# Performance work log

Measured on AMD Instinct MI355X. Metric: run time of the kernel, lower is better.

## Reference

```python
import jax, jax.numpy as jnp
import numpy as np

PS = 8          # patch_size
NF = 64         # num_feat
HEADS = 1
HW = 64         # hard-coded spatial size (Fold output_size=(64,64))
DIM = PS * PS * NF          # 4096
HID = DIM // HEADS          # 4096
NPATCH = (HW // PS) ** 2    # 64


def conv2d(x, w, b, groups=1):
    # x: [N,C,H,W], w: [O, C//groups, 3, 3], padding=1 stride=1 == SAME
    y = jax.lax.conv_general_dilated(
        x, w, window_strides=(1, 1), padding='SAME',
        dimension_numbers=('NCHW', 'OIHW', 'NCHW'),
        feature_group_count=groups)
    return y + b[None, :, None, None]


def unfold(x):
    # nn.Unfold(kernel=PS, stride=PS): [N,C,64,64] -> [N, C*PS*PS, NPATCH]
    N, C = x.shape[0], x.shape[1]
    g = HW // PS
    x = x.reshape(N, C, g, PS, g, PS)          # [N,C,gh,pi,gw,pj]
    x = x.transpose(0, 1, 3, 5, 2, 4)          # [N,C,pi,pj,gh,gw]
    return x.reshape(N, C * PS * PS, g * g)


def fold(y):
    # nn.Fold(output=(64,64), kernel=PS, stride=PS): inverse of unfold (non-overlapping)
    N = y.shape[0]
    g = HW // PS
    y = y.reshape(N, NF, PS, PS, g, g)         # [N,C,pi,pj,gh,gw]
    y = y.transpose(0, 1, 4, 2, 5, 3)          # [N,C,gh,pi,gw,pj]
    return y.reshape(N, NF, HW, HW)


def setup_inputs() -> dict:
    key = jax.random.key(0)
    ks = jax.random.split(key, 9)
    b, t = 4, 16
    x = jax.random.normal(ks[0], (b, t, NF, HW, HW), dtype=jnp.float32)
    s_dw = 1.0 / np.sqrt(9.0)          # depthwise: fan_in = 1*3*3
    s_fc = 1.0 / np.sqrt(NF * 9.0)     # full conv: fan_in = 64*3*3
    qw = jax.random.normal(ks[1], (NF, 1, 3, 3), jnp.float32) * s_dw
    qb = jax.random.normal(ks[2], (NF,), jnp.float32) * 0.01
    kw = jax.random.normal(ks[3], (NF, 1, 3, 3), jnp.float32) * s_dw
    kb = jax.random.normal(ks[4], (NF,), jnp.float32) * 0.01
    vw = jax.random.normal(ks[5], (NF, NF, 3, 3), jnp.float32) * s_fc
    vb = jax.random.normal(ks[6], (NF,), jnp.float32) * 0.01
    cw = jax.random.normal(ks[7], (NF, NF, 3, 3), jnp.float32) * s_fc
    cb = jax.random.normal(ks[8], (NF,), jnp.float32) * 0.01
    return {"x": x, "qw": qw, "qb": qb, "kw": kw, "kb": kb,
            "vw": vw, "vb": vb, "cw": cw, "cb": cb}


def reference(x, qw, qb, kw, kb, vw, vb, cw, cb):
    b, t, c, h, w = x.shape
    H, d, n = HEADS, HID, NPATCH
    xf = x.reshape(b * t, c, h, w)
    q = conv2d(xf, qw, qb, groups=NF)   # depthwise
    k = conv2d(xf, kw, kb, groups=NF)   # depthwise
    v = conv2d(xf, vw, vb)              # full conv
    # unfold -> [b,t,H,d,n] -> [b,H,d,t*n]
    def to_tokens(z):
        z = unfold(z).reshape(b, t, H, d, n)
        return z.transpose(0, 2, 3, 1, 4).reshape(b, H, d, t * n)
    uq, uk, uv = to_tokens(q), to_tokens(k), to_tokens(v)
    attn = jnp.einsum('bhdi,bhdj->bhij', uq, uk) * (d ** -0.5)
    attn = jax.nn.softmax(attn, axis=-1)
    ax = jnp.einsum('bhij,bhdj->bhid', attn, uv)          # [b,H,t*n,d]
    ax = ax.reshape(b, H, t, n, d).transpose(0, 2, 1, 4, 3)  # [b,t,H,d,n]
    ax = ax.reshape(b * t, DIM, n)
    feat = fold(ax)                                        # [b*t,C,64,64]
    out = conv2d(feat, cw, cb).reshape(x.shape)
    return out + x
```

## Files before the change

kernel.cpp:

```cpp
#include <hip/hip_runtime.h>

typedef unsigned short u16;
typedef unsigned int   u32;

typedef __bf16 bf16_t;
typedef bf16_t bf16x8 __attribute__((ext_vector_type(8)));
typedef float  f32x4  __attribute__((ext_vector_type(4)));

__device__ __forceinline__ float bf2f(u16 h) { return __uint_as_float(((u32)h) << 16); }
__device__ __forceinline__ u16 f2bf(float f) {
    u32 u = __float_as_uint(f);
    u32 r = u + 0x7fffu + ((u >> 16) & 1u);
    return (u16)(r >> 16);
}
__device__ __forceinline__ void unpack2(u32 v, float& a, float& b) {
    a = __uint_as_float(v << 16);
    b = __uint_as_float(v & 0xffff0000u);
}


__global__ __launch_bounds__(256) void dwconv_qk(
    const float* __restrict__ x, const float* __restrict__ qw, const float* __restrict__ qb,
    const float* __restrict__ kw, const float* __restrict__ kb,
    u16* __restrict__ qtok, u16* __restrict__ ktok)
{
    __shared__ float ts[64][65];
    int img = blockIdx.x >> 6, c = blockIdx.x & 63;
    int tid = threadIdx.x;
    const float* xp = x + ((size_t)((img << 6) + c) << 12);
    #pragma unroll
    for (int i = 0; i < 4; i++) {
        int p = i * 1024 + tid * 4;
        int r = p >> 6, col = p & 63;
        float4 v = *(const float4*)(xp + p);
        ts[r][col] = v.x; ts[r][col + 1] = v.y; ts[r][col + 2] = v.z; ts[r][col + 3] = v.w;
    }
    float qwv[9], kwv[9];
    #pragma unroll
    for (int i = 0; i < 9; i++) { qwv[i] = qw[c * 9 + i]; kwv[i] = kw[c * 9 + i]; }
    float qbb = qb[c], kbb = kb[c];
    __syncthreads();

    int r = tid >> 2, q = tid & 3;
    int b = img >> 4, t = img & 15;
    int gh = r >> 3, pr = r & 7;
    size_t base = (((size_t)(b << 10) + (t << 6) + (gh << 3)) << 12) + (c << 6) + (pr << 3);

    #pragma unroll
    for (int s = 0; s < 2; s++) {
        int gw = q * 2 + s, w0 = gw << 3;
        float qa[8], ka[8];
        #pragma unroll
        for (int i = 0; i < 8; i++) { qa[i] = qbb; ka[i] = kbb; }
        #pragma unroll
        for (int ky = 0; ky < 3; ky++) {
            int hh = r + ky - 1;
            if (hh < 0 || hh > 63) continue;
            float xr[10];
            #pragma unroll
            for (int cc = 0; cc < 10; cc++) {
                int ww = w0 - 1 + cc;
                xr[cc] = (ww < 0 || ww > 63) ? 0.f : ts[hh][ww];
            }
            #pragma unroll
            for (int kx = 0; kx < 3; kx++) {
                float wq = qwv[ky * 3 + kx], wk = kwv[ky * 3 + kx];
                #pragma unroll
                for (int i = 0; i < 8; i++) {
                    qa[i] += xr[i + kx] * wq;
                    ka[i] += xr[i + kx] * wk;
                }
            }
        }
        union { u16 h8[8]; uint4 u; } pq, pk;
        #pragma unroll
        for (int i = 0; i < 8; i++) { pq.h8[i] = f2bf(qa[i]); pk.h8[i] = f2bf(ka[i]); }
        size_t o = base + ((size_t)gw << 12);
        *(uint4*)&qtok[o] = pq.u;
        *(uint4*)&ktok[o] = pk.u;
    }
}

__global__ __launch_bounds__(256) void nchw_to_nhwc(
    const float* __restrict__ x, u16* __restrict__ xb)
{
    __shared__ float ts[64][65];
    int img = blockIdx.x >> 6, h = blockIdx.x & 63;
    int tid = threadIdx.x;
    const float* xp = x + ((size_t)img << 18) + (h << 6);
    int c = tid >> 2, wg = (tid & 3) << 4;
    #pragma unroll
    for (int i = 0; i < 4; i++) {
        float4 v = *(const float4*)(xp + ((size_t)c << 12) + wg + i * 4);
        ts[c][wg + i * 4 + 0] = v.x; ts[c][wg + i * 4 + 1] = v.y;
        ts[c][wg + i * 4 + 2] = v.z; ts[c][wg + i * 4 + 3] = v.w;
    }
    __syncthreads();
    int w = tid >> 2, cg = (tid & 3) << 4;
    union { u16 h8[8]; uint4 u; } p0, p1;
    #pragma unroll
    for (int m = 0; m < 8; m++) {
        p0.h8[m] = f2bf(ts[cg + m][w]);
        p1.h8[m] = f2bf(ts[cg + 8 + m][w]);
    }
    u16* dst = xb + (((((size_t)img << 6) + h) << 6) + w) * 64 + cg;
    *(uint4*)dst       = p0.u;
    *(uint4*)(dst + 8) = p1.u;
}

__global__ __launch_bounds__(256) void weight_prep2(
    const float* __restrict__ vw, const float* __restrict__ cw, u16* __restrict__ wt)
{
    int e = blockIdx.x * 256 + threadIdx.x;
    if (e >= 73728) return;
    int half = e >= 36864;
    int e2 = e - (half ? 36864 : 0);
    int tap = e2 >> 12;
    int kbg = (e2 >> 9) & 7;
    int cout = (e2 >> 3) & 63;
    int s = e2 & 7;
    int cin = (kbg << 3) + s;
    const float* src = half ? cw : vw;
    wt[e] = f2bf(src[((cout << 6) + cin) * 9 + tap]);
}

template<bool IS_C>
__global__ __launch_bounds__(256, 2) void conv_mfma(
    const u16* __restrict__ xb, const u16* __restrict__ wt,
    const float* __restrict__ bias, const float* __restrict__ xres,
    u16* __restrict__ vt, float* __restrict__ out)
{
    __shared__ u16 xs[21120];
    __shared__ u16 wl[18432];

    int tid = threadIdx.x, lane = tid & 63, wv = tid >> 6;
    int bid = blockIdx.x;
    int virt = (bid & 7) * 64 + (bid >> 3);
    int img = virt >> 3, rowblk = virt & 7;
    int h0 = rowblk << 3;
    int r16 = lane & 15, kb = lane >> 4;

    const uint4 z4 = make_uint4(0, 0, 0, 0);
    for (int i = tid; i < 80; i += 256) {
        int r = i >> 3, k = i & 7;
        *(uint4*)&xs[r * 2112 + 2048 + k * 8] = z4;
    }
    if (rowblk == 0)
        for (int i = tid; i < 264; i += 256) *(uint4*)&xs[i * 8] = z4;
    if (rowblk == 7)
        for (int i = tid; i < 264; i += 256) *(uint4*)&xs[9 * 2112 + i * 8] = z4;

    int pxoff[4][3];
    #pragma unroll
    for (int g = 0; g < 4; g++) {
        #pragma unroll
        for (int dx = 0; dx < 3; dx++) {
            int cc = g * 16 + r16 + dx - 1;
            int off;
            if (cc < 0)        off = 2048 + kb * 8;
            else if (cc >= 64) off = 2080 + kb * 8;
            else               off = (cc >> 4) * 512 + kb * 128 + (cc & 15) * 8;
            pxoff[g][dx] = off;
        }
    }

    const u16* xb_i = xb + ((size_t)img << 18);

    f32x4 acc[4][8] = {};

    for (int c0 = 0; c0 < 64; c0 += 32) {
        __syncthreads();
        #pragma unroll
        for (int k = 0; k < 10; k++) {
            int i = wv + (k << 2);
            int r = i >> 2, g = i & 3;
            int h = h0 + r - 1;
            if (h >= 0 && h < 64) {
                const u16* src = xb_i + (size_t)(((h << 6) + (g << 4) + r16) << 6)
                                 + c0 + (kb << 3);
                u16* dst = xs + r * 2112 + g * 512;
                __builtin_amdgcn_global_load_lds(
                    (const __attribute__((address_space(1))) u32*)src,
                    (__attribute__((address_space(3))) u32*)dst, 16, 0, 0);
            }
        }
        #pragma unroll
        for (int tp = 0; tp < 9; tp++) {
            const u16* srcw = wt + tp * 4096 + (c0 << 6) + tid * 8;
            u16* dstw = wl + tp * 2048 + (wv << 9);
            __builtin_amdgcn_global_load_lds(
                (const __attribute__((address_space(1))) u32*)srcw,
                (__attribute__((address_space(3))) u32*)dstw, 16, 0, 0);
        }
        __syncthreads();

        #pragma unroll
        for (int dy = 0; dy < 3; dy++) {
            #pragma unroll
            for (int dx = 0; dx < 3; dx++) {
                int tap = dy * 3 + dx;
                bf16x8 af[4];
                #pragma unroll
                for (int m = 0; m < 4; m++)
                    af[m] = *(const bf16x8*)&wl[tap * 2048 + (kb << 9)
                                                + (((m << 4) + r16) << 3)];
                #pragma unroll
                for (int nf = 0; nf < 8; nf++) {
                    int rowb = ((wv << 1) + (nf >> 2) + dy) * 2112;
                    bf16x8 bv = *(const bf16x8*)&xs[rowb + pxoff[nf & 3][dx]];
                    #pragma unroll
                    for (int m = 0; m < 4; m++)
                        acc[m][nf] = __builtin_amdgcn_mfma_f32_16x16x32_bf16(
                            af[m], bv, acc[m][nf], 0, 0, 0);
                }
            }
        }
    }

    int b = img >> 4, t = img & 15;
    if constexpr (!IS_C) {
        __syncthreads();
        u16* wbuf = xs + (wv << 12);
        int j0 = (t << 6) + (rowblk << 3);
        #pragma unroll
        for (int mh = 0; mh < 2; mh++) {
            #pragma unroll
            for (int mm = 0; mm < 2; mm++) {
                int m = mh * 2 + mm;
                #pragma unroll
                for (int q = 0; q < 4; q++) {
                    int cm = mm * 16 + (kb << 2) + q;
                    float bvs = bias[mh * 32 + cm];
                    #pragma unroll
                    for (int nf = 0; nf < 8; nf++) {
                        int lrL = nf >> 2;
                        int pc  = r16 & 7;
                        int gw  = ((nf & 3) << 1) | (r16 >> 3);
                        wbuf[(((cm << 1) | lrL) << 6) + (pc << 3) + gw] =
                            f2bf(acc[m][nf][q] + bvs);
                    }
                }
            }
            #pragma unroll
            for (int it = 0; it < 8; it++) {
                int cid = it * 64 + lane;
                int cm  = cid >> 4;
                int lrL = (cid >> 3) & 1;
                int pc  = cid & 7;
                int lr  = (wv << 1) | lrL;
                int cout = mh * 32 + cm;
                int dd  = (((lr << 3) | pc) << 6) | cout;
                uint4 val = *(uint4*)&wbuf[cid << 3];
                *(uint4*)&vt[(((size_t)((b << 12) + dd)) << 10) + j0] = val;
            }
            if (mh == 0) __syncthreads();
        }
    } else {
        #pragma unroll
        for (int m = 0; m < 4; m++) {
            #pragma unroll
            for (int q = 0; q < 4; q++) {
                int cout = (m << 4) + (kb << 2) + q;
                float bvs = bias[cout];
                #pragma unroll
                for (int nf = 0; nf < 8; nf++) {
                    int lr = (wv << 1) + (nf >> 2);
                    int w = (nf & 3) * 16 + r16;
                    int h = h0 + lr;
                    size_t o = ((size_t)((img << 6) + cout) << 12) + (h << 6) + w;
                    out[o] = acc[m][nf][q] + bvs + xres[o];
                }
            }
        }
    }
}

template<int TM, int TN, int LDA, int LDB, int LDC, int KTOT, int MT, int NT,
         int EPI, int OCC>
__global__ __launch_bounds__(256, OCC) void mfma_abt(
    const u16* __restrict__ Ag, const u16* __restrict__ Bg,
    float* __restrict__ rs, u16* __restrict__ Cg)
{
    constexpr int MF = TM / 32;
    constexpr int NF = TN / 32;
    constexpr int NWG = 4 * MT * NT;
    constexpr int CPX = NWG / 8;
    __shared__ u16 As[TM * 64];
    __shared__ u16 Bs[TN * 64];

    int tid  = threadIdx.x;
    int lane = tid & 63, wv = tid >> 6;
    int bid  = blockIdx.x;
    int id   = (bid & 7) * CPX + (bid >> 3);
    int nt   = id % NT;
    int rest = id / NT;
    int mt   = rest % MT;
    int bi   = rest / MT;

    const u16* Ab = Ag + (size_t)bi * (1024 * (size_t)LDA) + (size_t)(mt * TM) * LDA;
    const u16* Bb = Bg + (size_t)bi * ((size_t)NT * TN * LDB) + (size_t)(nt * TN) * LDB;

    int srow = tid >> 3;
    int slot = tid & 7;
    int wr = wv >> 1, wc = wv & 1;
    int r16 = lane & 15, kb = lane >> 4;

    f32x4 acc[MF][NF] = {};

    for (int k0 = 0; k0 < KTOT; k0 += 64) {
        __syncthreads();
        #pragma unroll
        for (int it = 0; it < MF; it++) {
            int rl = it * 32 + srow;
            int kg = slot ^ (rl & 7);
            const u16* sa = Ab + (size_t)rl * LDA + k0 + kg * 8;
            u16* da = As + it * 2048 + wv * 512;
            __builtin_amdgcn_global_load_lds(
                (const __attribute__((address_space(1))) u32*)sa,
                (__attribute__((address_space(3))) u32*)da, 16, 0, 0);
        }
        #pragma unroll
        for (int it = 0; it < NF; it++) {
            int rl = it * 32 + srow;
            int kg = slot ^ (rl & 7);
            const u16* sb = Bb + (size_t)rl * LDB + k0 + kg * 8;
            u16* db = Bs + it * 2048 + wv * 512;
            __builtin_amdgcn_global_load_lds(
                (const __attribute__((address_space(1))) u32*)sb,
                (__attribute__((address_space(3))) u32*)db, 16, 0, 0);
        }
        __syncthreads();

        #pragma unroll
        for (int kk = 0; kk < 2; kk++) {
            bf16x8 af[MF], bfr[NF];
            #pragma unroll
            for (int m = 0; m < MF; m++) {
                int row  = wr * (TM / 2) + m * 16 + r16;
                int boff = row * 128 + (((kk * 32 + kb * 8) * 2) ^ ((row & 7) << 4));
                af[m] = *(const bf16x8*)((const char*)As + boff);
            }
            #pragma unroll
            for (int n = 0; n < NF; n++) {
                int row  = wc * (TN / 2) + n * 16 + r16;
                int boff = row * 128 + (((kk * 32 + kb * 8) * 2) ^ ((row & 7) << 4));
                bfr[n] = *(const bf16x8*)((const char*)Bs + boff);
            }
            #pragma unroll
            for (int m = 0; m < MF; m++)
                #pragma unroll
                for (int n = 0; n < NF; n++)
                    acc[m][n] = __builtin_amdgcn_mfma_f32_16x16x32_bf16(
                        af[m], bfr[n], acc[m][n], 0, 0, 0);
        }
    }

    size_t crow0 = (size_t)bi * 1024 + (size_t)mt * TM + wr * (TM / 2);
    int col0 = nt * TN + wc * (TN / 2);
    if constexpr (EPI == 0) {
        #pragma unroll
        for (int m = 0; m < MF; m++) {
            #pragma unroll
            for (int q = 0; q < 4; q++) {
                size_t row = crow0 + m * 16 + kb * 4 + q;
                float rsum = 0.f;
                #pragma unroll
                for (int n = 0; n < NF; n++) {
                    float e = __expf(acc[m][n][q] * 0.015625f);
                    u16 pv = f2bf(e);
                    rsum += bf2f(pv);
                    Cg[row * (size_t)LDC + col0 + n * 16 + r16] = pv;
                }
                #pragma unroll
                for (int off = 1; off < 16; off <<= 1)
                    rsum += __shfl_xor(rsum, off);
                if (r16 == 0) atomicAdd(&rs[row], rsum);
            }
        }
    } else {
        #pragma unroll
        for (int m = 0; m < MF; m++) {
            float il[4];
            #pragma unroll
            for (int q = 0; q < 4; q++)
                il[q] = 1.0f / rs[crow0 + m * 16 + kb * 4 + q];
            #pragma unroll
            for (int n = 0; n < NF; n++) {
                #pragma unroll
                for (int q = 0; q < 4; q++) {
                    int i_loc = m * 16 + kb * 4 + q;
                    int j     = col0 + n * 16 + r16;
                    float v   = acc[m][n][q];
                    int i2 = mt * TM + wr * (TM / 2) + i_loc;
                    int t = i2 >> 6, patch = i2 & 63;
                    int c = j & 63, pr = (j >> 9) & 7, pc = (j >> 6) & 7;
                    int hh = ((patch >> 3) << 3) + pr, w2 = ((patch & 7) << 3) + pc;
                    size_t o = ((((size_t)(bi * 16 + t) << 6) + hh) << 6) + w2;
                    Cg[(o << 6) + c] = f2bf(v * il[q]);
                }
            }
        }
    }
}

extern "C" void kernel_launch(void* const* d_in, const int* in_sizes, int n_in,
                              void* d_out, int out_size, void* d_ws, size_t ws_size,
                              hipStream_t stream)
{
    const float* x  = (const float*)d_in[0];
    const float* qw = (const float*)d_in[1];
    const float* qb = (const float*)d_in[2];
    const float* kw = (const float*)d_in[3];
    const float* kb = (const float*)d_in[4];
    const float* vw = (const float*)d_in[5];
    const float* vb = (const float*)d_in[6];
    const float* cw = (const float*)d_in[7];
    const float* cb = (const float*)d_in[8];
    float* out = (float*)d_out;

    char* ws = (char*)d_ws;
    u16*   qtok  = (u16*)d_out;
    u16*   ktok  = (u16*)ws;
    u16*   probs = (u16*)(ws + (size_t)32 * 1024 * 1024);
    float* rowsum= (float*)(ws + (size_t)40 * 1024 * 1024);
    u16*   wtv   = (u16*)(ws + (size_t)40 * 1024 * 1024 + 65536);
    u16*   wtc   = wtv + 36864;
    u16*   xbuf  = ktok;
    u16*   vt    = qtok;
    u16*   axb   = ktok;

    weight_prep2<<<288, 256, 0, stream>>>(vw, cw, wtv);

    dwconv_qk<<<4096, 256, 0, stream>>>(x, qw, qb, kw, kb, qtok, ktok);

    hipMemsetAsync(rowsum, 0, 4096 * sizeof(float), stream);

    mfma_abt<64, 128, 4096, 4096, 1024, 4096, 16, 8, 0, 2><<<512, 256, 0, stream>>>(
        qtok, ktok, rowsum, probs);

    nchw_to_nhwc<<<4096, 256, 0, stream>>>(x, xbuf);

    conv_mfma<false><<<512, 256, 0, stream>>>(xbuf, wtv, vb, nullptr, vt, nullptr);

    mfma_abt<128, 128, 1024, 1024, 4096, 1024, 8, 32, 2, 4><<<1024, 256, 0, stream>>>(
        probs, vt, rowsum, axb);

    conv_mfma<true><<<512, 256, 0, stream>>>(axb, wtc, cb, x, nullptr, out);
}
```

Measured before the change: 302.4 us.

## Fold weight prep and rowsum clear into dwconv; widen QK GEMM K-tile

The weight-conversion kernel and the rowsum memset are merged into the first blocks of the depthwise conv kernel, removing two separate launches and their gaps on the stream. The GEMM template gains a BK parameter, and the QK^T GEMM now loads 128-wide K tiles instead of 64. That halves the number of loop iterations and barriers per tile, at the cost of more LDS per block. The extra work lands on some dwconv blocks, which makes those blocks slightly longer.

```diff
diff --git a/kernel.cpp b/kernel.cpp
--- a/kernel.cpp
+++ b/kernel.cpp
@@ -22,11 +22,30 @@
 __global__ __launch_bounds__(256) void dwconv_qk(
     const float* __restrict__ x, const float* __restrict__ qw, const float* __restrict__ qb,
     const float* __restrict__ kw, const float* __restrict__ kb,
-    u16* __restrict__ qtok, u16* __restrict__ ktok)
+    u16* __restrict__ qtok, u16* __restrict__ ktok,
+    const float* __restrict__ vw, const float* __restrict__ cw,
+    u16* __restrict__ wt, float* __restrict__ rowsum)
 {
     __shared__ float ts[64][65];
     int img = blockIdx.x >> 6, c = blockIdx.x & 63;
     int tid = threadIdx.x;
+
+    if (blockIdx.x < 288) {
+        int e = blockIdx.x * 256 + tid;
+        if (e < 73728) {
+            int half = e >= 36864;
+            int e2 = e - (half ? 36864 : 0);
+            int tap = e2 >> 12;
+            int kbg = (e2 >> 9) & 7;
+            int cout = (e2 >> 3) & 63;
+            int s = e2 & 7;
+            int cin = (kbg << 3) + s;
+            const float* src = half ? cw : vw;
+            wt[e] = f2bf(src[((cout << 6) + cin) * 9 + tap]);
+        }
+    }
+    if (blockIdx.x < 16) rowsum[blockIdx.x * 256 + tid] = 0.f;
+
     const float* xp = x + ((size_t)((img << 6) + c) << 12);
     #pragma unroll
     for (int i = 0; i < 4; i++) {
@@ -106,22 +125,6 @@
     u16* dst = xb + (((((size_t)img << 6) + h) << 6) + w) * 64 + cg;
     *(uint4*)dst       = p0.u;
     *(uint4*)(dst + 8) = p1.u;
-}
-
-__global__ __launch_bounds__(256) void weight_prep2(
-    const float* __restrict__ vw, const float* __restrict__ cw, u16* __restrict__ wt)
-{
-    int e = blockIdx.x * 256 + threadIdx.x;
-    if (e >= 73728) return;
-    int half = e >= 36864;
-    int e2 = e - (half ? 36864 : 0);
-    int tap = e2 >> 12;
-    int kbg = (e2 >> 9) & 7;
-    int cout = (e2 >> 3) & 63;
-    int s = e2 & 7;
-    int cin = (kbg << 3) + s;
-    const float* src = half ? cw : vw;
-    wt[e] = f2bf(src[((cout << 6) + cin) * 9 + tap]);
 }
 
 template<bool IS_C>
@@ -275,18 +278,22 @@
     }
 }
 
-template<int TM, int TN, int LDA, int LDB, int LDC, int KTOT, int MT, int NT,
-         int EPI, int OCC>
+template<int TM, int TN, int BK, int LDA, int LDB, int LDC, int KTOT, int MT,
+         int NT, int EPI, int OCC>
 __global__ __launch_bounds__(256, OCC) void mfma_abt(
     const u16* __restrict__ Ag, const u16* __restrict__ Bg,
     float* __restrict__ rs, u16* __restrict__ Cg)
 {
     constexpr int MF = TM / 32;
     constexpr int NF = TN / 32;
+    constexpr int SLOTS = BK / 8;
+    constexpr int AITS = TM * BK / 2048;
+    constexpr int BITS = TN * BK / 2048;
     constexpr int NWG = 4 * MT * NT;
     constexpr int CPX = NWG / 8;
-    __shared__ u16 As[TM * 64];
-    __shared__ u16 Bs[TN * 64];
+    constexpr int ROWSPP = 256 / SLOTS;
+    __shared__ u16 As[TM * BK];
+    __shared__ u16 Bs[TN * BK];
 
     int tid  = threadIdx.x;
     int lane = tid & 63, wv = tid >> 6;
@@ -300,18 +307,18 @@
     const u16* Ab = Ag + (size_t)bi * (1024 * (size_t)LDA) + (size_t)(mt * TM) * LDA;
     const u16* Bb = Bg + (size_t)bi * ((size_t)NT * TN * LDB) + (size_t)(nt * TN) * LDB;
 
-    int srow = tid >> 3;
-    int slot = tid & 7;
+    int srow = tid / SLOTS;
+    int slot = tid % SLOTS;
     int wr = wv >> 1, wc = wv & 1;
     int r16 = lane & 15, kb = lane >> 4;
 
     f32x4 acc[MF][NF] = {};
 
-    for (int k0 = 0; k0 < KTOT; k0 += 64) {
+    for (int k0 = 0; k0 < KTOT; k0 += BK) {
         __syncthreads();
         #pragma unroll
-        for (int it = 0; it < MF; it++) {
-            int rl = it * 32 + srow;
+        for (int it = 0; it < AITS; it++) {
+            int rl = it * ROWSPP + srow;
             int kg = slot ^ (rl & 7);
             const u16* sa = Ab + (size_t)rl * LDA + k0 + kg * 8;
             u16* da = As + it * 2048 + wv * 512;
@@ -320,8 +327,8 @@
                 (__attribute__((address_space(3))) u32*)da, 16, 0, 0);
         }
         #pragma unroll
-        for (int it = 0; it < NF; it++) {
-            int rl = it * 32 + srow;
+        for (int it = 0; it < BITS; it++) {
+            int rl = it * ROWSPP + srow;
             int kg = slot ^ (rl & 7);
             const u16* sb = Bb + (size_t)rl * LDB + k0 + kg * 8;
             u16* db = Bs + it * 2048 + wv * 512;
@@ -332,18 +339,18 @@
         __syncthreads();
 
         #pragma unroll
-        for (int kk = 0; kk < 2; kk++) {
+        for (int kk = 0; kk < BK / 32; kk++) {
             bf16x8 af[MF], bfr[NF];
             #pragma unroll
             for (int m = 0; m < MF; m++) {
                 int row  = wr * (TM / 2) + m * 16 + r16;
-                int boff = row * 128 + (((kk * 32 + kb * 8) * 2) ^ ((row & 7) << 4));
+                int boff = row * (2 * BK) + (((kk * 32 + kb * 8) * 2) ^ ((row & 7) << 4));
                 af[m] = *(const bf16x8*)((const char*)As + boff);
             }
             #pragma unroll
             for (int n = 0; n < NF; n++) {
                 int row  = wc * (TN / 2) + n * 16 + r16;
-                int boff = row * 128 + (((kk * 32 + kb * 8) * 2) ^ ((row & 7) << 4));
+                int boff = row * (2 * BK) + (((kk * 32 + kb * 8) * 2) ^ ((row & 7) << 4));
                 bfr[n] = *(const bf16x8*)((const char*)Bs + boff);
             }
             #pragma unroll
@@ -429,21 +436,18 @@
     u16*   vt    = qtok;
     u16*   axb   = ktok;
 
-    weight_prep2<<<288, 256, 0, stream>>>(vw, cw, wtv);
-
-    dwconv_qk<<<4096, 256, 0, stream>>>(x, qw, qb, kw, kb, qtok, ktok);
-
-    hipMemsetAsync(rowsum, 0, 4096 * sizeof(float), stream);
-
-    mfma_abt<64, 128, 4096, 4096, 1024, 4096, 16, 8, 0, 2><<<512, 256, 0, stream>>>(
-        qtok, ktok, rowsum, probs);
+    dwconv_qk<<<4096, 256, 0, stream>>>(x, qw, qb, kw, kb, qtok, ktok,
+                                        vw, cw, wtv, rowsum);
+
+    mfma_abt<64, 128, 128, 4096, 4096, 1024, 4096, 16, 8, 0, 2>
+        <<<512, 256, 0, stream>>>(qtok, ktok, rowsum, probs);
 
     nchw_to_nhwc<<<4096, 256, 0, stream>>>(x, xbuf);
 
     conv_mfma<false><<<512, 256, 0, stream>>>(xbuf, wtv, vb, nullptr, vt, nullptr);
 
-    mfma_abt<128, 128, 1024, 1024, 4096, 1024, 8, 32, 2, 4><<<1024, 256, 0, stream>>>(
-        probs, vt, rowsum, axb);
+    mfma_abt<128, 128, 64, 1024, 1024, 4096, 1024, 8, 32, 2, 4>
+        <<<1024, 256, 0, stream>>>(probs, vt, rowsum, axb);
 
     conv_mfma<true><<<512, 256, 0, stream>>>(axb, wtc, cb, x, nullptr, out);
 }
```

Measured after the change: 303.5 us. Within noise of the previous version (+0.4%).
